# Performance work log

Hardware: AMD Instinct MI355X
Metric: run time of the kernel (lower is better)

The kernel has to match this reference:

```python
import jax, jax.numpy as jnp
import numpy as np

BN_EPS = 1e-5

def setup_inputs() -> dict:
    key = jax.random.key(0)
    k_x, k_w, k_g, k_b, k_p = jax.random.split(key, 5)
    N, Cin, H, W = 32, 128, 56, 56
    Cout, K = 256, 3
    x = jax.random.normal(k_x, (N, Cin, H, W), dtype=jnp.float32)
    # random spatial permutation (Dconv_rand's torch.randperm(H*W))
    perm = jax.random.permutation(k_p, H * W).astype(jnp.int32)
    # conv weight, kaiming-ish scale
    w = jax.random.normal(k_w, (Cout, Cin, K, K), dtype=jnp.float32) * (2.0 / (Cin * K * K)) ** 0.5
    gamma = jnp.ones((Cout,), dtype=jnp.float32)
    beta = jnp.zeros((Cout,), dtype=jnp.float32)
    return {"x": x, "w": w, "gamma": gamma, "beta": beta, "perm": perm}


def reference(x, w, gamma, beta, perm):
    N, C, H, W = x.shape
    # Dconv_rand: randomly permute spatial positions, then standard 3x3 conv
    xp = x.reshape(N, C, H * W)[:, :, perm].reshape(N, C, H, W)
    y = jax.lax.conv_general_dilated(
        xp, w,
        window_strides=(1, 1),
        padding=((1, 1), (1, 1)),
        dimension_numbers=("NCHW", "OIHW", "NCHW"),
    )  # [N, Cout, H, W]
    # BatchNorm2d (training-mode batch stats, biased variance, eps=1e-5)
    mean = jnp.mean(y, axis=(0, 2, 3), keepdims=True)
    var = jnp.mean((y - mean) ** 2, axis=(0, 2, 3), keepdims=True)
    y_hat = (y - mean) * jax.lax.rsqrt(var + BN_EPS)
    out = y_hat * gamma.reshape(1, -1, 1, 1) + beta.reshape(1, -1, 1, 1)
    return jnp.maximum(out, 0.0)  # ReLU
```

## Files before the change

kernel.cpp:

```cpp
#include <hip/hip_runtime.h>
#include <hip/hip_bf16.h>
#include <stdint.h>

typedef __attribute__((ext_vector_type(8))) short bf16x8;
typedef __attribute__((ext_vector_type(4))) float f32x4;

#define N_IMG 32
#define CIN 128
#define COUT 256
#define HH 56
#define HW (HH*HH)
#define HP 58
#define PXTOT (N_IMG*HW)
#define NT 36

#define XP_BYTES    27557888u
#define WT_BYTES    589824u
#define INV_BYTES   12544u
#define STATS_BYTES 2048u
#define WS_MIN      (XP_BYTES + WT_BYTES + INV_BYTES + STATS_BYTES)
#define Y_BYTES     51380224u

__device__ __forceinline__ unsigned short f2bf(float f) {
  unsigned int u = __builtin_bit_cast(unsigned int, f);
  unsigned int r = u + 0x7FFFu + ((u >> 16) & 1u);
  return (unsigned short)(r >> 16);
}
__device__ __forceinline__ float bf2f(unsigned short s) {
  return __builtin_bit_cast(float, (unsigned int)s << 16);
}
__device__ __forceinline__ void gload_lds16(const void* g, void* l) {
  __builtin_amdgcn_global_load_lds((const __attribute__((address_space(1))) void*)g,
                                   (__attribute__((address_space(3))) void*)l, 16, 0, 0);
}

#define BAR()    __builtin_amdgcn_s_barrier()
#define WAITV4() asm volatile("s_waitcnt vmcnt(4)" ::: "memory")
#define WAITV0() asm volatile("s_waitcnt vmcnt(0)" ::: "memory")
#define WAITL()  asm volatile("s_waitcnt lgkmcnt(0)" ::: "memory")
#define SCHEDB() __builtin_amdgcn_sched_barrier(0)

__global__ __launch_bounds__(256) void wcvt_kernel(const float* __restrict__ w,
                                                   unsigned short* __restrict__ wt,
                                                   const int* __restrict__ perm,
                                                   int* __restrict__ inv,
                                                   float* __restrict__ stats) {
  int i = blockIdx.x * 256 + threadIdx.x;
  if (i < HW) inv[perm[i]] = i;
  if (i < 512) stats[i] = 0.f;
  if (i >= NT * COUT * 32) return;
  int kk = i >> 13;
  int r = i & 8191;
  int co = r >> 5, cl = r & 31;
  int o = kk >> 2, cb = kk & 3;
  int c = cb * 32 + cl;
  wt[i] = f2bf(w[(co * CIN + c) * 9 + o]);
}

__global__ __launch_bounds__(256) void pad_perm_kernel(const float* __restrict__ x,
                                                       const int* __restrict__ inv,
                                                       unsigned short* __restrict__ xp) {
  __shared__ unsigned short T[64 * 128];
  __shared__ int dest_off[64];
  int b = blockIdx.x;
  int n = b / 49;
  int k = b % 49;
  int s0 = k * 64;
  int t = threadIdx.x;

  if (t < 160) {
    int pi = k * 5 + (t >> 5);
    if (pi < 228) {
      int h, w2;
      if (pi < 58)       { h = 0;            w2 = pi; }
      else if (pi < 116) { h = 57;           w2 = pi - 58; }
      else if (pi < 172) { h = pi - 116 + 1; w2 = 0; }
      else               { h = pi - 172 + 1; w2 = 57; }
      uint2 z = {0u, 0u};
      *(uint2*)(xp + (size_t)((n * HP + h) * HP + w2) * CIN + (t & 31) * 4) = z;
    }
  }

  if (t < 64) {
    int s = inv[s0 + t];
    int h = s / HH, w = s % HH;
    dest_off[t] = ((n * HP + h + 1) * HP + (w + 1)) * CIN;
  }
  const float* xplane = x + (size_t)n * CIN * HW;
  #pragma unroll
  for (int i = 0; i < 32; ++i) {
    int idx = i * 256 + t;
    int c = idx >> 6, j = idx & 63;
    float v = xplane[c * HW + s0 + j];
    int byte = j * 256 + ((2 * c) ^ ((j & 7) << 4));
    *(unsigned short*)((char*)T + byte) = f2bf(v);
  }
  __syncthreads();
  #pragma unroll
  for (int i = 0; i < 4; ++i) {
    int u = i * 256 + t;
    int j = u >> 4, chunk = u & 15;
    int byte = j * 256 + ((chunk * 16) ^ ((j & 7) << 4));
    bf16x8 v = *(const bf16x8*)((const char*)T + byte);
    *(bf16x8*)(xp + dest_off[j] + chunk * 8) = v;
  }
}

template<int YMODE>
__global__ __launch_bounds__(256, 2) void conv_kernel(const unsigned short* __restrict__ xp,
                                                      const unsigned short* __restrict__ wt,
                                                      unsigned short* __restrict__ ybf,
                                                      float* __restrict__ yf32,
                                                      float* __restrict__ stats) {
  extern __shared__ unsigned short lds[];
  int t = threadIdx.x;
  int lane = t & 63, wid = t >> 6;
  int l = lane & 15, g = lane >> 4;
  int phys = blockIdx.x;
  int b = (phys & 7) * 98 + (phys >> 3);
  int pT = b >> 1;
  int coT = b & 1;
  int p0 = pT * 256;

  int lg = ((lane & 3) - (lane >> 3)) & 3;
  int aoff[2], adst[2];
  #pragma unroll
  for (int i = 0; i < 2; ++i) {
    int r = (wid * 2 + i) * 16 + (lane >> 2);
    aoff[i] = r * 32 + lg * 8;
    adst[i] = (wid * 2 + i) * 512 + lane * 8;
  }
  int bsrc[4], bdst[4];
  #pragma unroll
  for (int i = 0; i < 4; ++i) {
    int r = (wid * 4 + i) * 16 + (lane >> 2);
    int px = p0 + r;
    int n = px / HW, s = px % HW;
    int hi = s / HH, wi = s % HH;
    bsrc[i] = ((n * HP + hi) * HP + wi) * CIN + lg * 8;
    bdst[i] = 4096 + (wid * 4 + i) * 512 + lane * 8;
  }
  const unsigned short* wbase = wt + coT * 128 * 32;

  auto stageA = [&](int kt) {
    const unsigned short* s0 = wbase + kt * 8192;
    unsigned short* d = lds + (kt & 1) * 12288;
    gload_lds16(s0 + aoff[0], d + adst[0]);
    gload_lds16(s0 + aoff[1], d + adst[1]);
  };
  auto stageB = [&](int kt) {
    int o = kt >> 2, cb = kt & 3;
    int koff = ((o / 3) * HP + (o % 3)) * CIN + cb * 32;
    unsigned short* d = lds + (kt & 1) * 12288;
    #pragma unroll
    for (int i = 0; i < 4; ++i)
      gload_lds16(xp + bsrc[i] + koff, d + bdst[i]);
  };

  int pcs = ((g + (l >> 1)) & 3) * 8;
  int arow = l * 32 + pcs;
  int brow = 4096 + (wid * 64 + l) * 32 + pcs;

  bf16x8 afr[4], bfr[4];
  f32x4 acc[8][4];
  #pragma unroll
  for (int m = 0; m < 8; ++m)
    #pragma unroll
    for (int n = 0; n < 4; ++n) acc[m][n] = (f32x4)0.f;

#define LDA_H(MH) { _Pragma("unroll") for (int mm = 0; mm < 4; ++mm) \
    afr[mm] = *(const bf16x8*)(cur + arow + ((MH) * 4 + mm) * 16 * 32); }
#define LDB_ALL   { _Pragma("unroll") for (int nn = 0; nn < 4; ++nn) \
    bfr[nn] = *(const bf16x8*)(cur + brow + nn * 16 * 32); }
#define MFMA_H(MB) { _Pragma("unroll") for (int mm = 0; mm < 4; ++mm) \
    _Pragma("unroll") for (int nn = 0; nn < 4; ++nn) \
      acc[(MB)+mm][nn] = __builtin_amdgcn_mfma_f32_16x16x32_bf16(afr[mm], bfr[nn], acc[(MB)+mm][nn], 0, 0, 0); }

  stageA(0);
  stageB(0);
  stageB(1);
  WAITV4();
  BAR();

  #pragma unroll 1
  for (int kt = 0; kt < NT; ++kt) {
    const unsigned short* cur = lds + (kt & 1) * 12288;
    bool st1 = (kt + 1) < NT;
    bool st2 = (kt + 2) < NT;
    LDA_H(0); LDB_ALL;
    if (st1) stageA(kt + 1);
    BAR();
    WAITL(); SCHEDB();
    __builtin_amdgcn_s_setprio(1);
    MFMA_H(0);
    __builtin_amdgcn_s_setprio(0);
    BAR();
    LDA_H(1);
    if (st2) stageB(kt + 2);
    BAR();
    WAITL(); SCHEDB();
    __builtin_amdgcn_s_setprio(1);
    MFMA_H(4);
    __builtin_amdgcn_s_setprio(0);
    if (st2) { WAITV4(); } else if (st1) { WAITV0(); }
    BAR();
  }
#undef LDA_H
#undef LDB_ALL
#undef MFMA_H

  float ps1[8][4], ps2[8][4];
  #pragma unroll
  for (int m = 0; m < 8; ++m)
    #pragma unroll
    for (int j = 0; j < 4; ++j) {
      float a = 0.f, b2 = 0.f;
      #pragma unroll
      for (int n = 0; n < 4; ++n) { float v = acc[m][n][j]; a += v; b2 += v * v; }
      #pragma unroll
      for (int off = 1; off < 16; off <<= 1) {
        a  += __shfl_xor(a, off, 64);
        b2 += __shfl_xor(b2, off, 64);
      }
      ps1[m][j] = a; ps2[m][j] = b2;
    }

  #pragma unroll
  for (int n = 0; n < 4; ++n) {
    int px = p0 + wid * 64 + n * 16 + l;
    if (YMODE == 1) {
      #pragma unroll
      for (int m = 0; m < 8; ++m) {
        int co = coT * 128 + m * 16 + g * 4;
        #pragma unroll
        for (int j = 0; j < 4; ++j)
          ybf[(size_t)(co + j) * PXTOT + px] = f2bf(acc[m][n][j]);
      }
    } else {
      int nimg = px / HW, s = px % HW;
      float* obase = yf32 + (size_t)nimg * COUT * HW + s;
      #pragma unroll
      for (int m = 0; m < 8; ++m) {
        int co = coT * 128 + m * 16 + g * 4;
        #pragma unroll
        for (int j = 0; j < 4; ++j)
          obase[(size_t)(co + j) * HW] = acc[m][n][j];
      }
    }
  }

  float* sb = (float*)lds;
  if (l == 0) {
    #pragma unroll
    for (int m = 0; m < 8; ++m)
      #pragma unroll
      for (int j = 0; j < 4; ++j) {
        int cl = m * 16 + g * 4 + j;
        sb[cl * 4 + wid] = ps1[m][j];
        sb[512 + cl * 4 + wid] = ps2[m][j];
      }
  }
  BAR();
  if (t < 128) {
    int co = coT * 128 + t;
    float a  = sb[t * 4] + sb[t * 4 + 1] + sb[t * 4 + 2] + sb[t * 4 + 3];
    float b2 = sb[512 + t * 4] + sb[512 + t * 4 + 1] + sb[512 + t * 4 + 2] + sb[512 + t * 4 + 3];
    atomicAdd(&stats[co], a);
    atomicAdd(&stats[256 + co], b2);
  }
}

__global__ __launch_bounds__(256) void bnrelu1_kernel(const unsigned short* __restrict__ y,
                                                      const float* __restrict__ stats,
                                                      const float* __restrict__ gamma,
                                                      const float* __restrict__ beta,
                                                      float* __restrict__ out) {
  int idx = blockIdx.x * 256 + threadIdx.x;
  const int UN = PXTOT / 8;
  int co = idx / UN;
  int rem = idx - co * UN;
  float cnt = (float)PXTOT;
  float mean = stats[co] / cnt;
  float var = stats[256 + co] / cnt - mean * mean;
  float sc = gamma[co] * rsqrtf(var + 1e-5f);
  float sh = beta[co] - mean * sc;
  bf16x8 v = *(const bf16x8*)(y + (size_t)co * PXTOT + rem * 8);
  int px0 = rem * 8;
  int n = px0 / HW, s = px0 - n * HW;
  float* o = out + ((size_t)n * COUT + co) * HW + s;
  float4 r0, r1;
  r0.x = fmaxf(bf2f((unsigned short)v[0]) * sc + sh, 0.f);
  r0.y = fmaxf(bf2f((unsigned short)v[1]) * sc + sh, 0.f);
  r0.z = fmaxf(bf2f((unsigned short)v[2]) * sc + sh, 0.f);
  r0.w = fmaxf(bf2f((unsigned short)v[3]) * sc + sh, 0.f);
  r1.x = fmaxf(bf2f((unsigned short)v[4]) * sc + sh, 0.f);
  r1.y = fmaxf(bf2f((unsigned short)v[5]) * sc + sh, 0.f);
  r1.z = fmaxf(bf2f((unsigned short)v[6]) * sc + sh, 0.f);
  r1.w = fmaxf(bf2f((unsigned short)v[7]) * sc + sh, 0.f);
  ((float4*)o)[0] = r0;
  ((float4*)o)[1] = r1;
}

__global__ __launch_bounds__(256) void bnrelu0_kernel(float* __restrict__ y,
                                                      const float* __restrict__ stats,
                                                      const float* __restrict__ gamma,
                                                      const float* __restrict__ beta) {
  int idx = blockIdx.x * 256 + threadIdx.x;
  int plane = idx / (HW / 4);
  int co = plane & 255;
  float cnt = (float)PXTOT;
  float mean = stats[co] / cnt;
  float var = stats[256 + co] / cnt - mean * mean;
  float sc = gamma[co] * rsqrtf(var + 1e-5f);
  float sh = beta[co] - mean * sc;
  float4 v = ((float4*)y)[idx];
  v.x = fmaxf(v.x * sc + sh, 0.f);
  v.y = fmaxf(v.y * sc + sh, 0.f);
  v.z = fmaxf(v.z * sc + sh, 0.f);
  v.w = fmaxf(v.w * sc + sh, 0.f);
  ((float4*)y)[idx] = v;
}

extern "C" void kernel_launch(void* const* d_in, const int* in_sizes, int n_in,
                              void* d_out, int out_size, void* d_ws, size_t ws_size,
                              hipStream_t stream) {
  const float* x     = (const float*)d_in[0];
  const float* w     = (const float*)d_in[1];
  const float* gamma = (const float*)d_in[2];
  const float* beta  = (const float*)d_in[3];
  const int*   perm  = (const int*)d_in[4];
  float* out = (float*)d_out;
  char* ws = (char*)d_ws;

  unsigned short* xp = (unsigned short*)ws;
  unsigned short* wt = (unsigned short*)(ws + XP_BYTES);
  int* inv           = (int*)(ws + XP_BYTES + WT_BYTES);
  float* stats       = (float*)(ws + XP_BYTES + WT_BYTES + INV_BYTES);
  unsigned short* y  = (unsigned short*)(ws + WS_MIN);
  bool ymode = ws_size >= (size_t)WS_MIN + Y_BYTES;

  hipFuncSetAttribute(reinterpret_cast<const void*>(conv_kernel<1>),
                      hipFuncAttributeMaxDynamicSharedMemorySize, 49152);
  hipFuncSetAttribute(reinterpret_cast<const void*>(conv_kernel<0>),
                      hipFuncAttributeMaxDynamicSharedMemorySize, 49152);

  wcvt_kernel<<<1152, 256, 0, stream>>>(w, wt, perm, inv, stats);
  pad_perm_kernel<<<N_IMG * 49, 256, 0, stream>>>(x, inv, xp);
  if (ymode) {
    conv_kernel<1><<<784, 256, 49152, stream>>>(xp, wt, y, out, stats);
    bnrelu1_kernel<<<COUT * (PXTOT / 8) / 256, 256, 0, stream>>>(y, stats, gamma, beta, out);
  } else {
    conv_kernel<0><<<784, 256, 49152, stream>>>(xp, wt, (unsigned short*)out, out, stats);
    bnrelu0_kernel<<<N_IMG * COUT * HW / 4 / 256, 256, 0, stream>>>(out, stats, gamma, beta);
  }
}
```

Baseline: 123.6 us.

## Triple-buffer B tiles in LDS and merge the two MFMA halves per k-step

The conv GEMM main loop now splits LDS into a double-buffered A region and a triple-buffered B region, so the B prefetch for step kt+2 can be issued together with the A prefetch at the start of each iteration. It also loads all eight A fragments at once and runs a single MFMA block per k-step instead of two halves separated by barriers. This halves the barriers per iteration and gives the global-to-LDS loads more time to overlap compute. The cost is more LDS per block (64 KB instead of 48 KB) and more live A-fragment registers, which may reduce occupancy.

```diff
diff --git a/kernel.cpp b/kernel.cpp
--- a/kernel.cpp
+++ b/kernel.cpp
@@ -138,20 +138,20 @@
     int n = px / HW, s = px % HW;
     int hi = s / HH, wi = s % HH;
     bsrc[i] = ((n * HP + hi) * HP + wi) * CIN + lg * 8;
-    bdst[i] = 4096 + (wid * 4 + i) * 512 + lane * 8;
+    bdst[i] = (wid * 4 + i) * 512 + lane * 8;
   }
   const unsigned short* wbase = wt + coT * 128 * 32;
 
   auto stageA = [&](int kt) {
     const unsigned short* s0 = wbase + kt * 8192;
-    unsigned short* d = lds + (kt & 1) * 12288;
+    unsigned short* d = lds + (kt & 1) * 4096;
     gload_lds16(s0 + aoff[0], d + adst[0]);
     gload_lds16(s0 + aoff[1], d + adst[1]);
   };
-  auto stageB = [&](int kt) {
+  auto stageB = [&](int kt, int buf) {
     int o = kt >> 2, cb = kt & 3;
     int koff = ((o / 3) * HP + (o % 3)) * CIN + cb * 32;
-    unsigned short* d = lds + (kt & 1) * 12288;
+    unsigned short* d = lds + 8192 + buf * 8192;
     #pragma unroll
     for (int i = 0; i < 4; ++i)
       gload_lds16(xp + bsrc[i] + koff, d + bdst[i]);
@@ -159,55 +159,52 @@
 
   int pcs = ((g + (l >> 1)) & 3) * 8;
   int arow = l * 32 + pcs;
-  int brow = 4096 + (wid * 64 + l) * 32 + pcs;
-
-  bf16x8 afr[4], bfr[4];
+  int brow = (wid * 64 + l) * 32 + pcs;
+
+  bf16x8 afr[8], bfr[4];
   f32x4 acc[8][4];
   #pragma unroll
   for (int m = 0; m < 8; ++m)
     #pragma unroll
     for (int n = 0; n < 4; ++n) acc[m][n] = (f32x4)0.f;
 
-#define LDA_H(MH) { _Pragma("unroll") for (int mm = 0; mm < 4; ++mm) \
-    afr[mm] = *(const bf16x8*)(cur + arow + ((MH) * 4 + mm) * 16 * 32); }
-#define LDB_ALL   { _Pragma("unroll") for (int nn = 0; nn < 4; ++nn) \
-    bfr[nn] = *(const bf16x8*)(cur + brow + nn * 16 * 32); }
-#define MFMA_H(MB) { _Pragma("unroll") for (int mm = 0; mm < 4; ++mm) \
+#define LDA_ALL { _Pragma("unroll") for (int mm = 0; mm < 8; ++mm) \
+    afr[mm] = *(const bf16x8*)(curA + arow + mm * 16 * 32); }
+#define LDB_ALL { _Pragma("unroll") for (int nn = 0; nn < 4; ++nn) \
+    bfr[nn] = *(const bf16x8*)(curB + brow + nn * 16 * 32); }
+#define MFMA_ALL { _Pragma("unroll") for (int mm = 0; mm < 8; ++mm) \
     _Pragma("unroll") for (int nn = 0; nn < 4; ++nn) \
-      acc[(MB)+mm][nn] = __builtin_amdgcn_mfma_f32_16x16x32_bf16(afr[mm], bfr[nn], acc[(MB)+mm][nn], 0, 0, 0); }
+      acc[mm][nn] = __builtin_amdgcn_mfma_f32_16x16x32_bf16(afr[mm], bfr[nn], acc[mm][nn], 0, 0, 0); }
 
   stageA(0);
-  stageB(0);
-  stageB(1);
+  stageB(0, 0);
+  stageB(1, 1);
   WAITV4();
   BAR();
 
+  int pb = 0;
   #pragma unroll 1
   for (int kt = 0; kt < NT; ++kt) {
-    const unsigned short* cur = lds + (kt & 1) * 12288;
+    const unsigned short* curA = lds + (kt & 1) * 4096;
+    const unsigned short* curB = lds + 8192 + pb * 8192;
     bool st1 = (kt + 1) < NT;
     bool st2 = (kt + 2) < NT;
-    LDA_H(0); LDB_ALL;
+    int pb2 = pb + 2; if (pb2 >= 3) pb2 -= 3;
+    LDA_ALL; LDB_ALL;
     if (st1) stageA(kt + 1);
+    if (st2) stageB(kt + 2, pb2);
     BAR();
     WAITL(); SCHEDB();
     __builtin_amdgcn_s_setprio(1);
-    MFMA_H(0);
-    __builtin_amdgcn_s_setprio(0);
-    BAR();
-    LDA_H(1);
-    if (st2) stageB(kt + 2);
-    BAR();
-    WAITL(); SCHEDB();
-    __builtin_amdgcn_s_setprio(1);
-    MFMA_H(4);
+    MFMA_ALL;
     __builtin_amdgcn_s_setprio(0);
     if (st2) { WAITV4(); } else if (st1) { WAITV0(); }
     BAR();
-  }
-#undef LDA_H
+    pb = (pb + 1 == 3) ? 0 : pb + 1;
+  }
+#undef LDA_ALL
 #undef LDB_ALL
-#undef MFMA_H
+#undef MFMA_ALL
 
   float ps1[8][4], ps2[8][4];
   #pragma unroll
@@ -340,17 +337,17 @@
   bool ymode = ws_size >= (size_t)WS_MIN + Y_BYTES;
 
   hipFuncSetAttribute(reinterpret_cast<const void*>(conv_kernel<1>),
-                      hipFuncAttributeMaxDynamicSharedMemorySize, 49152);
+                      hipFuncAttributeMaxDynamicSharedMemorySize, 65536);
   hipFuncSetAttribute(reinterpret_cast<const void*>(conv_kernel<0>),
-                      hipFuncAttributeMaxDynamicSharedMemorySize, 49152);
+                      hipFuncAttributeMaxDynamicSharedMemorySize, 65536);
 
   wcvt_kernel<<<1152, 256, 0, stream>>>(w, wt, perm, inv, stats);
   pad_perm_kernel<<<N_IMG * 49, 256, 0, stream>>>(x, inv, xp);
   if (ymode) {
-    conv_kernel<1><<<784, 256, 49152, stream>>>(xp, wt, y, out, stats);
+    conv_kernel<1><<<784, 256, 65536, stream>>>(xp, wt, y, out, stats);
     bnrelu1_kernel<<<COUT * (PXTOT / 8) / 256, 256, 0, stream>>>(y, stats, gamma, beta, out);
   } else {
-    conv_kernel<0><<<784, 256, 49152, stream>>>(xp, wt, (unsigned short*)out, out, stats);
+    conv_kernel<0><<<784, 256, 65536, stream>>>(xp, wt, (unsigned short*)out, out, stats);
     bnrelu0_kernel<<<N_IMG * COUT * HW / 4 / 256, 256, 0, stream>>>(out, stats, gamma, beta);
   }
 }
```

Result: no change. 121.9 us (median of 2 runs) (-1.4%).
